# Kernel optimization log

Hardware: AMD Instinct MI355X
Metric: run time of the kernel (lower is better)

Reference implementation:

```python
import jax, jax.numpy as jnp
import numpy as np


def _transition_matrix(durations, max_seq_len):
    # durations: (B, L_enc) int; returns (B, L_enc, L_dec) float32
    rng = jnp.arange(max_seq_len)                         # (L_dec,)
    cs = jnp.cumsum(durations, axis=1)[..., None]         # (B, L_enc, 1)
    mask1 = rng < cs
    # torch .roll(1) without dim flattens -> roll -> reshape; jnp.roll(axis=None) matches
    shifted = jnp.roll(durations, 1)
    shifted = shifted.at[:, 0].set(0)
    cs2 = jnp.cumsum(shifted, axis=1)[..., None]
    mask2 = rng < cs2
    tm = mask1 & (~mask2)
    return tm.astype(jnp.float32)


def setup_inputs() -> dict:
    key = jax.random.key(0)
    k1, k2 = jax.random.split(key)
    B, L_enc, E = 32, 512, 256
    L_dec = 2048
    encoder_output = jax.random.normal(k1, (B, L_enc, E), dtype=jnp.float32)
    durations = jax.random.randint(k2, (B, L_enc), 0, 8, dtype=jnp.int64)
    return {
        "encoder_output": encoder_output,
        "durations": durations,
        "decoder_max_seq_len": L_dec,
    }


def reference(encoder_output, durations, decoder_max_seq_len):
    tm = _transition_matrix(durations, decoder_max_seq_len)   # (B, L_enc, L_dec)
    # bmm(enc^T, tm)^T  ==  einsum over L_enc
    return jnp.einsum("ble,bld->bde", encoder_output, tm)     # (B, L_dec, E)
```

## Files before the change

### kernel.cpp

```cpp
#include <hip/hip_runtime.h>

#define B_    32
#define LENC  512
#define LDEC  2048
#define E4    64
#define TPB   256
#define NWAVE (TPB / 64)
#define ROWS_PER_BLOCK 16
#define ROWS_PER_WAVE  (ROWS_PER_BLOCK / NWAVE)

__global__ __launch_bounds__(TPB) void length_regulator_fused(
    const float4* __restrict__ enc, const int2* __restrict__ dur2,
    float4* __restrict__ out) {
  const int t    = threadIdx.x;
  const int lane = t & 63;
  const int wid  = t >> 6;
  const int b    = blockIdx.y;

  __shared__ int cs[LENC];
  __shared__ int wsum[NWAVE];

  const int2 v = dur2[b * (LENC / 2) + t];
  int x = v.x + v.y;
#pragma unroll
  for (int off = 1; off < 64; off <<= 1) {
    const int y = __shfl_up(x, off, 64);
    if (lane >= off) x += y;
  }
  if (lane == 63) wsum[wid] = x;
  __syncthreads();
  int wo = 0;
#pragma unroll
  for (int w = 0; w < NWAVE; ++w) wo += (w < wid) ? wsum[w] : 0;
  const int ip = x + wo;
  cs[2 * t + 1] = ip;
  cs[2 * t]     = ip - v.y;
  __syncthreads();

  const int total = cs[LENC - 1];
  const int d0 = blockIdx.x * ROWS_PER_BLOCK + wid * ROWS_PER_WAVE;

  int lo = 0, hi = LENC;
  while (lo < hi) {
    const int mid = (lo + hi) >> 1;
    if (cs[mid] <= d0) lo = mid + 1; else hi = mid;
  }

  int los[ROWS_PER_WAVE];
#pragma unroll
  for (int r = 0; r < ROWS_PER_WAVE; ++r) {
    while (lo < LENC && cs[lo] <= d0 + r) ++lo;
    los[r] = lo;
  }

  const size_t enc_base = (size_t)b * LENC * E4 + lane;
  const size_t out_base = (size_t)b * LDEC * E4 + (size_t)d0 * E4 + lane;

  float4 vals[ROWS_PER_WAVE];
#pragma unroll
  for (int r = 0; r < ROWS_PER_WAVE; ++r) {
    vals[r] = make_float4(0.f, 0.f, 0.f, 0.f);
    if (d0 + r < total)
      vals[r] = enc[enc_base + (size_t)los[r] * E4];
  }
#pragma unroll
  for (int r = 0; r < ROWS_PER_WAVE; ++r)
    out[out_base + (size_t)r * E4] = vals[r];
}

extern "C" void kernel_launch(void* const* d_in, const int* in_sizes, int n_in,
                              void* d_out, int out_size, void* d_ws, size_t ws_size,
                              hipStream_t stream) {
  const float* enc = (const float*)d_in[0];
  const int*   dur = (const int*)d_in[1];

  dim3 grid(LDEC / ROWS_PER_BLOCK, B_);
  length_regulator_fused<<<grid, TPB, 0, stream>>>(
      (const float4*)enc, (const int2*)dur, (float4*)d_out);
}
```

Baseline: 87.66 us.

## Split into segment-index precompute kernel and batch-interleaved gather kernel

Moves the per-batch prefix sum and the row-to-encoder-index binary search out of the gather kernel. A small build_seg kernel writes a per-decoder-row source index (or -1 for padding) into workspace, and a lean gather kernel reads four indices with one int4 load. The gather grid is flattened with the batch index as the fastest dimension. Previously each of the 4096 blocks redid the 512-element scan. The new path adds a second launch and a serialized 32-block prologue kernel.

```diff
diff --git a/kernel.cpp b/kernel.cpp
--- a/kernel.cpp
+++ b/kernel.cpp
@@ -8,6 +8,77 @@
 #define NWAVE (TPB / 64)
 #define ROWS_PER_BLOCK 16
 #define ROWS_PER_WAVE  (ROWS_PER_BLOCK / NWAVE)
+
+
+__global__ __launch_bounds__(TPB) void build_seg(
+    const int2* __restrict__ dur2, int* __restrict__ seg) {
+  const int b    = blockIdx.x;
+  const int t    = threadIdx.x;
+  const int lane = t & 63;
+  const int wid  = t >> 6;
+
+  __shared__ int cs[LENC];
+  __shared__ int wsum[NWAVE];
+
+  const int2 v = dur2[b * (LENC / 2) + t];
+  int x = v.x + v.y;
+#pragma unroll
+  for (int off = 1; off < 64; off <<= 1) {
+    const int y = __shfl_up(x, off, 64);
+    if (lane >= off) x += y;
+  }
+  if (lane == 63) wsum[wid] = x;
+  __syncthreads();
+  int wo = 0;
+#pragma unroll
+  for (int w = 0; w < NWAVE; ++w) wo += (w < wid) ? wsum[w] : 0;
+  const int ip = x + wo;
+  cs[2 * t + 1] = ip;
+  cs[2 * t]     = ip - v.y;
+  __syncthreads();
+
+  const int total = cs[LENC - 1];
+
+  for (int i = t; i < LDEC; i += TPB) {
+    int lo = 0, hi = LENC;
+#pragma unroll
+    for (int s = 0; s < 10; ++s) {
+      const int mid = (lo + hi) >> 1;
+      if (mid < LENC && cs[mid] <= i) lo = mid + 1; else hi = mid;
+    }
+    seg[b * LDEC + i] = (i < total) ? lo : -1;
+  }
+}
+
+__global__ __launch_bounds__(TPB) void gather(
+    const float4* __restrict__ enc, const int* __restrict__ seg,
+    float4* __restrict__ out) {
+  const int g     = blockIdx.x;
+  const int b     = g & 31;
+  const int chunk = g >> 5;
+  const int t     = threadIdx.x;
+  const int lane  = t & 63;
+  const int wid   = t >> 6;
+
+  const int d0 = chunk * ROWS_PER_BLOCK + wid * ROWS_PER_WAVE;
+
+  const int4 s4 = *reinterpret_cast<const int4*>(&seg[b * LDEC + d0]);
+  const int ls[ROWS_PER_WAVE] = {s4.x, s4.y, s4.z, s4.w};
+
+  const size_t enc_base = (size_t)b * LENC * E4 + lane;
+  const size_t out_base = (size_t)b * LDEC * E4 + (size_t)d0 * E4 + lane;
+
+  float4 vals[ROWS_PER_WAVE];
+#pragma unroll
+  for (int r = 0; r < ROWS_PER_WAVE; ++r) {
+    vals[r] = make_float4(0.f, 0.f, 0.f, 0.f);
+    if (ls[r] >= 0)
+      vals[r] = enc[enc_base + (size_t)ls[r] * E4];
+  }
+#pragma unroll
+  for (int r = 0; r < ROWS_PER_WAVE; ++r)
+    out[out_base + (size_t)r * E4] = vals[r];
+}
 
 __global__ __launch_bounds__(TPB) void length_regulator_fused(
     const float4* __restrict__ enc, const int2* __restrict__ dur2,
@@ -74,7 +145,15 @@
   const float* enc = (const float*)d_in[0];
   const int*   dur = (const int*)d_in[1];
 
-  dim3 grid(LDEC / ROWS_PER_BLOCK, B_);
-  length_regulator_fused<<<grid, TPB, 0, stream>>>(
-      (const float4*)enc, (const int2*)dur, (float4*)d_out);
+  const size_t seg_bytes = (size_t)B_ * LDEC * sizeof(int);
+  if (ws_size >= seg_bytes && d_ws != nullptr) {
+    int* seg = (int*)d_ws;
+    build_seg<<<dim3(B_), TPB, 0, stream>>>((const int2*)dur, seg);
+    gather<<<dim3((LDEC / ROWS_PER_BLOCK) * B_), TPB, 0, stream>>>(
+        (const float4*)enc, seg, (float4*)d_out);
+  } else {
+    dim3 grid(LDEC / ROWS_PER_BLOCK, B_);
+    length_regulator_fused<<<grid, TPB, 0, stream>>>(
+        (const float4*)enc, (const int2*)dur, (float4*)d_out);
+  }
 }
```

Measured after the change: 93.24 us. 1.06x slower.
